# Kernel tuning notes

Hardware: AMD Instinct MI355X
Metric: run time of the kernel (lower is better)

## Reference

```python
import jax, jax.numpy as jnp
import numpy as np

B, S, D, H = 4, 1024, 1024, 16
HD = D // H  # head_dim = 64


def setup_inputs() -> dict:
    key = jax.random.key(0)
    ks = jax.random.split(key, 16)
    w = lambda k: jax.random.normal(k, (D, D), dtype=jnp.float32) * 0.02
    b = lambda k: jax.random.normal(k, (D,), dtype=jnp.float32) * 0.02
    x = jax.random.normal(ks[0], (B, S, D), dtype=jnp.float32)
    mask = jnp.tril(jnp.ones((S, S), dtype=jnp.int32))[None, None]  # causal [1,1,S,S]
    bar_indices = jax.random.randint(ks[1], (S,), 0, S, dtype=jnp.int64)
    beat_indices = jax.random.randint(ks[2], (S,), 0, S, dtype=jnp.int64)
    return {
        "x": x, "mask": mask, "bar_indices": bar_indices, "beat_indices": beat_indices,
        "Wq": w(ks[3]), "bq": b(ks[4]), "Wk": w(ks[5]), "bk": b(ks[6]),
        "Wv": w(ks[7]), "bv": b(ks[8]),
        "W_bark": w(ks[9]), "b_bark": b(ks[10]),
        "W_beatk": w(ks[11]), "b_beatk": b(ks[12]),
        "Wo": w(ks[13]), "bo": b(ks[14]),
    }


def reference(x, mask, bar_indices, beat_indices, Wq, bq, Wk, bk, Wv, bv,
              W_bark, b_bark, W_beatk, b_beatk, Wo, bo):
    Bs, Sl, Dm = x.shape
    heads, hd = H, Dm // H

    def proj(t, W, b):  # torch Linear: t @ W.T + b, then split heads -> [B,H,S,hd]
        y = t @ W.T + b
        return y.reshape(Bs, -1, heads, hd).transpose(0, 2, 1, 3)

    q = proj(x, Wq, bq)
    k = proj(x, Wk, bk)
    v = proj(x, Wv, bv)
    scale = 1.0 / jnp.sqrt(jnp.asarray(hd, x.dtype))

    scores = jnp.einsum('bhqd,bhkd->bhqk', q, k) * scale

    # hierarchical bar bias (bar_query is computed but unused in the original)
    bar_k = proj(x[:, bar_indices], W_bark, b_bark)
    scores = scores + 0.2 * (jnp.einsum('bhqd,bhkd->bhqk', q, bar_k) * scale)

    # hierarchical beat bias
    beat_k = proj(x[:, beat_indices], W_beatk, b_beatk)
    scores = scores + 0.1 * (jnp.einsum('bhqd,bhkd->bhqk', q, beat_k) * scale)

    scores = jnp.where(mask == 0, jnp.asarray(-1e9, scores.dtype), scores)
    attn = jax.nn.softmax(scores, axis=-1)  # dropout is identity in eval

    out = jnp.einsum('bhqk,bhkd->bhqd', attn, v)
    out = out.transpose(0, 2, 1, 3).reshape(Bs, Sl, Dm)
    return out @ Wo.T + bo
```

## Files before the change

kernel.cpp:

```cpp
#include <hip/hip_runtime.h>
#include <hip/hip_bf16.h>


typedef __bf16 bf16x8 __attribute__((ext_vector_type(8)));
typedef __bf16 bf16x4 __attribute__((ext_vector_type(4)));
typedef float  f32x4  __attribute__((ext_vector_type(4)));

#define DMODEL 1024

#define ASYNC_LOAD16(gp, lp)                                                  \
    __builtin_amdgcn_global_load_lds(                                         \
        (const __attribute__((address_space(1))) unsigned int*)(gp),          \
        (__attribute__((address_space(3))) unsigned int*)(lp), 16, 0, 0)

__global__ __launch_bounds__(256) void cvt_kernel(
    const float* __restrict__ x,
    const float* __restrict__ Wq, const float* __restrict__ Wk,
    const float* __restrict__ Wv, const float* __restrict__ Wbar,
    const float* __restrict__ Wbeat, const float* __restrict__ Wo,
    __bf16* __restrict__ dst)
{
    const int g = blockIdx.x * 256 + threadIdx.x;
    const size_t e = (size_t)g * 8;
    const int seg = (int)(e >> 20);
    const float* src; size_t off; float s = 1.0f;
    if (seg < 4)       { src = x;     off = e; }
    else if (seg == 4) { src = Wq;    off = e - ((size_t)4 << 20); }
    else if (seg == 5) { src = Wk;    off = e - ((size_t)5 << 20); }
    else if (seg == 6) { src = Wv;    off = e - ((size_t)6 << 20); }
    else if (seg == 7) { src = Wbar;  off = e - ((size_t)7 << 20); s = 0.2f; }
    else if (seg == 8) { src = Wbeat; off = e - ((size_t)8 << 20); s = 0.1f; }
    else               { src = Wo;    off = e - ((size_t)9 << 20); }
    const float4 a = *(const float4*)&src[off];
    const float4 b = *(const float4*)&src[off + 4];
    bf16x8 v;
    v[0] = (__bf16)(a.x * s); v[1] = (__bf16)(a.y * s);
    v[2] = (__bf16)(a.z * s); v[3] = (__bf16)(a.w * s);
    v[4] = (__bf16)(b.x * s); v[5] = (__bf16)(b.y * s);
    v[6] = (__bf16)(b.z * s); v[7] = (__bf16)(b.w * s);
    *(bf16x8*)&dst[e] = v;
}


#define SWZ_COL(r_, ks_) \
    (((((ks_) * 64) + quad * 16) ^ (((r_) & 7) << 4)) >> 1)

#define READ_ALL(c_)                                                          \
    do {                                                                      \
        _Pragma("unroll") for (int mh = 0; mh < 2; ++mh)                      \
        _Pragma("unroll") for (int mi = 0; mi < 2; ++mi) {                    \
            const int r_ = ((w >> 2) << 5) + mh * 64 + mi * 16 + l15;         \
            _Pragma("unroll") for (int ks = 0; ks < 2; ++ks)                  \
                af[mh][mi][ks] = *(const bf16x8*)&Alds[(c_) * 8192 +          \
                                        r_ * 64 + SWZ_COL(r_, ks)];           \
        }                                                                     \
        _Pragma("unroll") for (int nh = 0; nh < 2; ++nh)                      \
        _Pragma("unroll") for (int nj = 0; nj < 2; ++nj) {                    \
            const int r_ = ((w & 3) << 5) + nh * 128 + nj * 16 + l15;         \
            _Pragma("unroll") for (int ks = 0; ks < 2; ++ks)                  \
                bfr[nh][nj][ks] = *(const bf16x8*)&Blds[(c_) * 16384 +        \
                                        r_ * 64 + SWZ_COL(r_, ks)];           \
        }                                                                     \
    } while (0)

#define STAGE_A1(bufn_, h_, kt_)                                              \
    do {                                                                      \
        const int tm_ = (kt_) >> 4;                                           \
        const int k0_ = ((kt_) & 15) << 6;                                    \
        const __bf16* ap_ = (tm_ == 0) ? aA0##h_ : (tm_ == 1) ? aA1##h_       \
                                                              : aA2##h_;      \
        ASYNC_LOAD16(ap_ + k0_,                                               \
                     &Alds[(bufn_) * 8192 + (h_) * 4096 + w * 512]);          \
    } while (0)

#define STAGE_B2(bufn_, h_, kt_)                                              \
    do {                                                                      \
        const int tm_ = (kt_) >> 4;                                           \
        const int k0_ = ((kt_) & 15) << 6;                                    \
        const __bf16* wp_ = (tm_ == 0) ? W0 : (tm_ == 1) ? W1 : W2;           \
        ASYNC_LOAD16(wp_ + bro##h_##0 + k0_,                                  \
                     &Blds[(bufn_) * 16384 + (h_) * 8192 + w * 512]);         \
        ASYNC_LOAD16(wp_ + bro##h_##1 + k0_,                                  \
                     &Blds[(bufn_) * 16384 + (h_) * 8192 + 4096 + w * 512]);  \
    } while (0)

#define PHASE_BAR1()                                                          \
    do {                                                                      \
        __builtin_amdgcn_s_barrier();                                         \
        asm volatile("s_waitcnt lgkmcnt(0)" ::: "memory");                    \
    } while (0)

#define MFMA16(nh_)                                                           \
    do {                                                                      \
        __builtin_amdgcn_s_setprio(1);                                        \
        _Pragma("unroll") for (int mh = 0; mh < 2; ++mh)                      \
        _Pragma("unroll") for (int mi = 0; mi < 2; ++mi)                      \
        _Pragma("unroll") for (int nj = 0; nj < 2; ++nj)                      \
        _Pragma("unroll") for (int ks = 0; ks < 2; ++ks) {                    \
            acc[mh * 2 + mi][(nh_) * 2 + nj] =                                \
                __builtin_amdgcn_mfma_f32_16x16x32_bf16(                      \
                    af[mh][mi][ks], bfr[(nh_)][nj][ks],                       \
                    acc[mh * 2 + mi][(nh_) * 2 + nj], 0, 0, 0);               \
        }                                                                     \
        __builtin_amdgcn_s_setprio(0);                                        \
    } while (0)

__global__ __launch_bounds__(512, 2) void gemm8p_kernel(
    const __bf16* __restrict__ xb,
    const __bf16* __restrict__ Wqb, const __bf16* __restrict__ Wkb,
    const __bf16* __restrict__ Wvb, const __bf16* __restrict__ Wbarb,
    const __bf16* __restrict__ Wbeatb,
    const float* __restrict__ bq, const float* __restrict__ bk,
    const float* __restrict__ bv, const float* __restrict__ bbar,
    const float* __restrict__ bbeat,
    const int* __restrict__ bar_idx, const int* __restrict__ beat_idx,
    __bf16* __restrict__ qbuf, __bf16* __restrict__ keffbuf,
    __bf16* __restrict__ vtbuf)
{
    __shared__ __align__(16) __bf16 Alds[3 * 8192];
    __shared__ __align__(16) __bf16 Blds[3 * 16384];

    const int bid = blockIdx.x;
    int mode, tk;
    if (bid < 128)      { mode = 1; tk = bid; }
    else if (bid < 256) { mode = 0; tk = bid - 128; }
    else                { mode = 2; tk = bid - 256; }
    const int m0 = (tk >> 2) << 7;
    const int n0 = (tk & 3) << 8;
    const int nkt = (mode == 1) ? 48 : 16;

    const int t    = (int)threadIdx.x;
    const int w    = t >> 6;
    const int lane = t & 63;
    const int l15  = lane & 15;
    const int quad = lane >> 4;

    const int srow = t >> 3;
    const int scol = ((((t & 7) * 16) ^ (((t >> 3) & 7) << 4)) >> 1);

    const __bf16* aA00 = xb + (size_t)(m0 + srow) * DMODEL + scol;
    const __bf16* aA01 = xb + (size_t)(m0 + 64 + srow) * DMODEL + scol;
    const __bf16* aA10 = aA00; const __bf16* aA11 = aA01;
    const __bf16* aA20 = aA00; const __bf16* aA21 = aA01;
    const __bf16 *W0, *W1, *W2;
    if (mode == 0)      { W0 = W1 = W2 = Wqb; }
    else if (mode == 2) { W0 = W1 = W2 = Wvb; }
    else {
        W0 = Wkb; W1 = Wbarb; W2 = Wbeatb;
        const int bb = m0 & ~1023;
        const int lr = m0 & 1023;
        aA10 = xb + (size_t)(bb + bar_idx[lr + srow]) * DMODEL + scol;
        aA11 = xb + (size_t)(bb + bar_idx[lr + 64 + srow]) * DMODEL + scol;
        aA20 = xb + (size_t)(bb + beat_idx[lr + srow]) * DMODEL + scol;
        aA21 = xb + (size_t)(bb + beat_idx[lr + 64 + srow]) * DMODEL + scol;
    }
    const size_t bro00 = (size_t)(n0 + srow) * DMODEL + scol;
    const size_t bro01 = (size_t)(n0 + 64 + srow) * DMODEL + scol;
    const size_t bro10 = (size_t)(n0 + 128 + srow) * DMODEL + scol;
    const size_t bro11 = (size_t)(n0 + 192 + srow) * DMODEL + scol;

    f32x4 acc[4][4];
#pragma unroll
    for (int i = 0; i < 4; ++i)
#pragma unroll
        for (int j = 0; j < 4; ++j)
            acc[i][j] = {0.f, 0.f, 0.f, 0.f};
    bf16x8 af[2][2][2], bfr[2][2][2];

    STAGE_A1(0, 0, 0);
    STAGE_A1(0, 1, 0);
    STAGE_B2(0, 0, 0);
    STAGE_B2(0, 1, 0);
    asm volatile("" ::: "memory");
    STAGE_A1(1, 0, 1);
    STAGE_A1(1, 1, 1);
    STAGE_B2(1, 0, 1);
    STAGE_B2(1, 1, 1);
    asm volatile("s_waitcnt vmcnt(6)" ::: "memory");
    __builtin_amdgcn_s_barrier();

    int rc = 0, fc = 2;
#pragma unroll 1
    for (int kt = 0; kt < nkt; ++kt) {
        const int kn = kt + 2;
        const bool st = (kn < nkt);

        READ_ALL(rc);
        if (st) { STAGE_A1(fc, 0, kn); STAGE_A1(fc, 1, kn); }
        PHASE_BAR1();
        MFMA16(0);

        if (st) { STAGE_B2(fc, 0, kn); STAGE_B2(fc, 1, kn); }
        if (kt < nkt - 2)
            asm volatile("s_waitcnt vmcnt(6)" ::: "memory");
        else if (kt == nkt - 2)
            asm volatile("s_waitcnt vmcnt(0)" ::: "memory");
        PHASE_BAR1();
        MFMA16(1);

        rc = (rc == 2) ? 0 : rc + 1;
        fc = (fc == 2) ? 0 : fc + 1;
    }

#pragma unroll
    for (int an = 0; an < 4; ++an) {
        const int col = n0 + ((w & 3) << 5) + (an >> 1) * 128 +
                        (an & 1) * 16 + l15;
        float bias;
        if (mode == 0)      bias = bq[col];
        else if (mode == 1) bias = bk[col] + 0.2f * bbar[col] + 0.1f * bbeat[col];
        else                bias = bv[col];
#pragma unroll
        for (int am = 0; am < 4; ++am) {
            const int rowbase = m0 + ((w >> 2) << 5) + (am >> 1) * 64 +
                                (am & 1) * 16 + quad * 4;
            if (mode == 2) {
                const int bb = rowbase >> 10;
                const int sb = rowbase & 1023;
                bf16x4 vv;
#pragma unroll
                for (int r = 0; r < 4; ++r) vv[r] = (__bf16)(acc[am][an][r] + bias);
                *(bf16x4*)&vtbuf[((size_t)(bb * 1024 + col)) * 1024 + sb] = vv;
            } else if (mode == 0) {
#pragma unroll
                for (int r = 0; r < 4; ++r)
                    qbuf[(size_t)(rowbase + r) * DMODEL + col] =
                        (__bf16)((acc[am][an][r] + bias) * 0.125f);
            } else {
#pragma unroll
                for (int r = 0; r < 4; ++r)
                    keffbuf[(size_t)(rowbase + r) * DMODEL + col] =
                        (__bf16)(acc[am][an][r] + bias);
            }
        }
    }
}

__global__ __launch_bounds__(256) void oproj_kernel(
    const __bf16* __restrict__ attnb, const __bf16* __restrict__ Wob,
    const float* __restrict__ bo, float* __restrict__ outb)
{
    const int tile = blockIdx.x;
    const int m0 = (tile >> 3) << 6;
    const int n0 = (tile & 7) << 7;

    __shared__ __align__(16) __bf16 Alds[64 * 32];
    __shared__ __align__(16) __bf16 Blds[128 * 32];

    const int t    = threadIdx.x;
    const int w    = t >> 6;
    const int lane = t & 63;
    const int l15  = lane & 15;
    const int quad = lane >> 4;
    const int wm   = (w >> 1) << 5;
    const int wn   = (w & 1) << 6;
    const int srow = t >> 2;
    const int scol = ((((t & 3) * 16) ^ (((t >> 2) & 3) << 4)) >> 1);
    const int rcol = (((quad * 16) ^ ((l15 & 3) << 4)) >> 1);

    const __bf16* gA  = attnb + (size_t)(m0 + srow) * DMODEL + scol;
    const __bf16* gB0 = Wob + (size_t)(n0 + srow) * DMODEL + scol;
    const __bf16* gB1 = Wob + (size_t)(n0 + 64 + srow) * DMODEL + scol;
    __bf16* lA  = &Alds[w * 512];
    __bf16* lB0 = &Blds[w * 512];
    __bf16* lB1 = &Blds[2048 + w * 512];

    f32x4 acc[2][4];
    for (int i = 0; i < 2; ++i)
        for (int j = 0; j < 4; ++j)
            acc[i][j] = {0.f, 0.f, 0.f, 0.f};

    for (int kk = 0; kk < 32; ++kk) {
        const int k0 = kk * 32;
        ASYNC_LOAD16(gA + k0, lA);
        ASYNC_LOAD16(gB0 + k0, lB0);
        ASYNC_LOAD16(gB1 + k0, lB1);
        __syncthreads();

        bf16x8 af[2], bfr[4];
        for (int i = 0; i < 2; ++i)
            af[i] = *(const bf16x8*)&Alds[(wm + i * 16 + l15) * 32 + rcol];
        for (int j = 0; j < 4; ++j)
            bfr[j] = *(const bf16x8*)&Blds[(wn + j * 16 + l15) * 32 + rcol];

        for (int i = 0; i < 2; ++i)
            for (int j = 0; j < 4; ++j)
                acc[i][j] = __builtin_amdgcn_mfma_f32_16x16x32_bf16(
                    af[i], bfr[j], acc[i][j], 0, 0, 0);
        __syncthreads();
    }

    for (int j = 0; j < 4; ++j) {
        const int col = n0 + wn + j * 16 + l15;
        const float bias = bo[col];
        for (int i = 0; i < 2; ++i) {
            const int rowbase = m0 + wm + i * 16 + quad * 4;
            for (int r = 0; r < 4; ++r)
                outb[(size_t)(rowbase + r) * DMODEL + col] = acc[i][j][r] + bias;
        }
    }
}

__global__ __launch_bounds__(256) void attn_kernel(
    const __bf16* __restrict__ qbuf, const __bf16* __restrict__ keffbuf,
    const __bf16* __restrict__ vtbuf, __bf16* __restrict__ attnbuf)
{
    const int bh = blockIdx.y;
    const int b  = bh >> 4;
    const int h  = bh & 15;
    const int qt = blockIdx.x;
    const int q0 = qt * 64;

    __shared__ __align__(16) __bf16 Klds[64][72];
    __shared__ __align__(16) __bf16 Vlds[64][72];
    __shared__ __align__(16) __bf16 Plds[4][16][72];

    const int t    = threadIdx.x;
    const int w    = t >> 6;
    const int lane = t & 63;
    const int l15  = lane & 15;
    const int quad = lane >> 4;

    const __bf16* qbase =
        qbuf + (size_t)(b * 1024 + q0 + w * 16 + l15) * DMODEL + h * 64;
    bf16x8 qf0 = *(const bf16x8*)&qbase[quad * 8];
    bf16x8 qf1 = *(const bf16x8*)&qbase[32 + quad * 8];

    bf16x8 ones;
    for (int i = 0; i < 8; ++i) ones[i] = (__bf16)1.0f;

    f32x4 o[4];
    for (int i = 0; i < 4; ++i) o[i] = {0.f, 0.f, 0.f, 0.f};
    f32x4 lacc = {0.f, 0.f, 0.f, 0.f};

    const int srow = t >> 2;
    const int scol = (t & 3) * 16;

    const __bf16* kbase = keffbuf + (size_t)(b * 1024) * DMODEL + h * 64;
    const __bf16* vtb   = vtbuf + (size_t)(b * 1024 + h * 64) * 1024;

    for (int j = 0; j <= qt; ++j) {
        const __bf16* kg = kbase + (size_t)(j * 64 + srow) * DMODEL + scol;
        *(bf16x8*)&Klds[srow][scol]     = *(const bf16x8*)kg;
        *(bf16x8*)&Klds[srow][scol + 8] = *(const bf16x8*)(kg + 8);
        const __bf16* vg = vtb + (size_t)srow * 1024 + j * 64 + scol;
        *(bf16x8*)&Vlds[srow][scol]     = *(const bf16x8*)vg;
        *(bf16x8*)&Vlds[srow][scol + 8] = *(const bf16x8*)(vg + 8);
        __syncthreads();

        f32x4 sc[4];
        for (int nt = 0; nt < 4; ++nt) {
            sc[nt] = {0.f, 0.f, 0.f, 0.f};
            bf16x8 kf0 = *(const bf16x8*)&Klds[nt * 16 + l15][quad * 8];
            bf16x8 kf1 = *(const bf16x8*)&Klds[nt * 16 + l15][32 + quad * 8];
            sc[nt] = __builtin_amdgcn_mfma_f32_16x16x32_bf16(qf0, kf0, sc[nt], 0, 0, 0);
            sc[nt] = __builtin_amdgcn_mfma_f32_16x16x32_bf16(qf1, kf1, sc[nt], 0, 0, 0);
        }

        if (j == qt) {
            const int qrow_base = q0 + w * 16 + quad * 4;
            for (int nt = 0; nt < 4; ++nt) {
                const int kcol = j * 64 + nt * 16 + l15;
                for (int r = 0; r < 4; ++r)
                    if (kcol > qrow_base + r) sc[nt][r] = -1e30f;
            }
        }

        for (int nt = 0; nt < 4; ++nt)
            for (int r = 0; r < 4; ++r)
                sc[nt][r] = __expf(sc[nt][r]);

        for (int nt = 0; nt < 4; ++nt)
            for (int r = 0; r < 4; ++r)
                Plds[w][quad * 4 + r][nt * 16 + l15] = (__bf16)sc[nt][r];
        asm volatile("s_waitcnt lgkmcnt(0)" ::: "memory");

        bf16x8 pf0 = *(const bf16x8*)&Plds[w][l15][quad * 8];
        bf16x8 pf1 = *(const bf16x8*)&Plds[w][l15][32 + quad * 8];

        lacc = __builtin_amdgcn_mfma_f32_16x16x32_bf16(pf0, ones, lacc, 0, 0, 0);
        lacc = __builtin_amdgcn_mfma_f32_16x16x32_bf16(pf1, ones, lacc, 0, 0, 0);

        for (int nd = 0; nd < 4; ++nd) {
            bf16x8 vf0 = *(const bf16x8*)&Vlds[nd * 16 + l15][quad * 8];
            bf16x8 vf1 = *(const bf16x8*)&Vlds[nd * 16 + l15][32 + quad * 8];
            o[nd] = __builtin_amdgcn_mfma_f32_16x16x32_bf16(pf0, vf0, o[nd], 0, 0, 0);
            o[nd] = __builtin_amdgcn_mfma_f32_16x16x32_bf16(pf1, vf1, o[nd], 0, 0, 0);
        }
        __syncthreads();
    }

    float rinv[4];
    for (int r = 0; r < 4; ++r) rinv[r] = 1.0f / lacc[r];
    for (int nd = 0; nd < 4; ++nd) {
        for (int r = 0; r < 4; ++r) {
            const int row = q0 + w * 16 + quad * 4 + r;
            attnbuf[(size_t)(b * 1024 + row) * DMODEL + h * 64 + nd * 16 + l15] =
                (__bf16)(o[nd][r] * rinv[r]);
        }
    }
}

extern "C" void kernel_launch(void* const* d_in, const int* in_sizes, int n_in,
                              void* d_out, int out_size, void* d_ws, size_t ws_size,
                              hipStream_t stream) {
    const float* x     = (const float*)d_in[0];
    const int* bar     = (const int*)d_in[2];
    const int* beat    = (const int*)d_in[3];
    const float* Wq    = (const float*)d_in[4];
    const float* bq    = (const float*)d_in[5];
    const float* Wk    = (const float*)d_in[6];
    const float* bk    = (const float*)d_in[7];
    const float* Wv    = (const float*)d_in[8];
    const float* bv    = (const float*)d_in[9];
    const float* Wbar  = (const float*)d_in[10];
    const float* bbar  = (const float*)d_in[11];
    const float* Wbeat = (const float*)d_in[12];
    const float* bbeat = (const float*)d_in[13];
    const float* Wo    = (const float*)d_in[14];
    const float* bo    = (const float*)d_in[15];

    const size_t M1 = (size_t)1 << 20;
    __bf16* xb     = (__bf16*)d_ws;
    __bf16* Wqb    = xb + 4 * M1;
    __bf16* Wkb    = Wqb + M1;
    __bf16* Wvb    = Wkb + M1;
    __bf16* Wbarb  = Wvb + M1;
    __bf16* Wbeatb = Wbarb + M1;
    __bf16* Wob    = Wbeatb + M1;
    __bf16* qbuf   = Wob + M1;
    __bf16* keff   = qbuf + 4 * M1;
    __bf16* vt     = keff + 4 * M1;
    __bf16* attn   = vt + 4 * M1;
    float*  outb   = (float*)d_out;

    cvt_kernel<<<5120, 256, 0, stream>>>(x, Wq, Wk, Wv, Wbar, Wbeat, Wo, xb);

    gemm8p_kernel<<<384, 512, 0, stream>>>(
        xb, Wqb, Wkb, Wvb, Wbarb, Wbeatb,
        bq, bk, bv, bbar, bbeat, bar, beat,
        qbuf, keff, vt);

    attn_kernel<<<dim3(16, 64), 256, 0, stream>>>(qbuf, keff, vt, attn);

    oproj_kernel<<<512, 256, 0, stream>>>(attn, Wob, bo, outb);
}
```

Measured before the change: 221.5 us.

## Double-buffer attention K/V tiles with async LDS loads and 128-row query blocks

Rewrites the attention kernel to use 512-thread blocks covering 128 query rows, so each K/V tile loaded is shared by twice as many query rows. K/V tiles now go straight from global memory into LDS through global_load_lds, with two buffers so the next tile streams in while the current one is computed. The LDS layout uses an XOR swizzle to avoid bank conflicts. Blocks are ordered so heavy and light causal query tiles are interleaved across the grid. The trade-offs are more LDS per block, fewer blocks (512), and hand-placed waitcnt/barrier logic that must stay correct.

```diff
diff --git a/kernel.cpp b/kernel.cpp
--- a/kernel.cpp
+++ b/kernel.cpp
@@ -301,76 +301,98 @@
     }
 }
 
-__global__ __launch_bounds__(256) void attn_kernel(
+#define ATT_SLOT(q_, r_) ((((q_) ^ ((r_) & 7))) * 8)
+
+__global__ __launch_bounds__(512) void attn_kernel(
     const __bf16* __restrict__ qbuf, const __bf16* __restrict__ keffbuf,
     const __bf16* __restrict__ vtbuf, __bf16* __restrict__ attnbuf)
 {
-    const int bh = blockIdx.y;
+    const int id = blockIdx.x;
+    const int bh = id & 63;
     const int b  = bh >> 4;
     const int h  = bh & 15;
-    const int qt = blockIdx.x;
-    const int q0 = qt * 64;
-
-    __shared__ __align__(16) __bf16 Klds[64][72];
-    __shared__ __align__(16) __bf16 Vlds[64][72];
-    __shared__ __align__(16) __bf16 Plds[4][16][72];
-
-    const int t    = threadIdx.x;
+    const int qr = id >> 6;
+    const int qt = (qr < 4) ? qr : 11 - qr;
+    const int q0 = qt << 7;
+    const int NT = 2 * qt + 2;
+
+    __shared__ __align__(16) __bf16 Klds[2][64 * 64];
+    __shared__ __align__(16) __bf16 Vlds[2][64 * 64];
+    __shared__ __align__(16) __bf16 Plds[8][16][72];
+
+    const int t    = (int)threadIdx.x;
     const int w    = t >> 6;
     const int lane = t & 63;
     const int l15  = lane & 15;
     const int quad = lane >> 4;
 
+    const int srow = t >> 3;
+    const int scol = ((t & 7) ^ (srow & 7)) * 8;
+
+    const __bf16* gK = keffbuf + (size_t)(b * 1024 + srow) * DMODEL +
+                       h * 64 + scol;
+    const __bf16* gV = vtbuf + (size_t)(b * 1024 + h * 64 + srow) * 1024 +
+                       scol;
+
     const __bf16* qbase =
         qbuf + (size_t)(b * 1024 + q0 + w * 16 + l15) * DMODEL + h * 64;
     bf16x8 qf0 = *(const bf16x8*)&qbase[quad * 8];
     bf16x8 qf1 = *(const bf16x8*)&qbase[32 + quad * 8];
 
     bf16x8 ones;
+#pragma unroll
     for (int i = 0; i < 8; ++i) ones[i] = (__bf16)1.0f;
 
     f32x4 o[4];
+#pragma unroll
     for (int i = 0; i < 4; ++i) o[i] = {0.f, 0.f, 0.f, 0.f};
     f32x4 lacc = {0.f, 0.f, 0.f, 0.f};
 
-    const int srow = t >> 2;
-    const int scol = (t & 3) * 16;
-
-    const __bf16* kbase = keffbuf + (size_t)(b * 1024) * DMODEL + h * 64;
-    const __bf16* vtb   = vtbuf + (size_t)(b * 1024 + h * 64) * 1024;
-
-    for (int j = 0; j <= qt; ++j) {
-        const __bf16* kg = kbase + (size_t)(j * 64 + srow) * DMODEL + scol;
-        *(bf16x8*)&Klds[srow][scol]     = *(const bf16x8*)kg;
-        *(bf16x8*)&Klds[srow][scol + 8] = *(const bf16x8*)(kg + 8);
-        const __bf16* vg = vtb + (size_t)srow * 1024 + j * 64 + scol;
-        *(bf16x8*)&Vlds[srow][scol]     = *(const bf16x8*)vg;
-        *(bf16x8*)&Vlds[srow][scol + 8] = *(const bf16x8*)(vg + 8);
-        __syncthreads();
+    ASYNC_LOAD16(gK, &Klds[0][t * 8]);
+    ASYNC_LOAD16(gV, &Vlds[0][t * 8]);
+    asm volatile("" ::: "memory");
+    ASYNC_LOAD16(gK + (size_t)64 * DMODEL, &Klds[1][t * 8]);
+    ASYNC_LOAD16(gV + 64, &Vlds[1][t * 8]);
+    asm volatile("s_waitcnt vmcnt(2)" ::: "memory");
+    __builtin_amdgcn_s_barrier();
+
+#pragma unroll 1
+    for (int j = 0; j < NT; ++j) {
+        const int cur = j & 1;
 
         f32x4 sc[4];
+#pragma unroll
         for (int nt = 0; nt < 4; ++nt) {
+            const int row = nt * 16 + l15;
+            bf16x8 kf0 = *(const bf16x8*)&Klds[cur][row * 64 +
+                                                    ATT_SLOT(quad, row)];
+            bf16x8 kf1 = *(const bf16x8*)&Klds[cur][row * 64 +
+                                                    ATT_SLOT(quad + 4, row)];
             sc[nt] = {0.f, 0.f, 0.f, 0.f};
-            bf16x8 kf0 = *(const bf16x8*)&Klds[nt * 16 + l15][quad * 8];
-            bf16x8 kf1 = *(const bf16x8*)&Klds[nt * 16 + l15][32 + quad * 8];
             sc[nt] = __builtin_amdgcn_mfma_f32_16x16x32_bf16(qf0, kf0, sc[nt], 0, 0, 0);
             sc[nt] = __builtin_amdgcn_mfma_f32_16x16x32_bf16(qf1, kf1, sc[nt], 0, 0, 0);
         }
 
-        if (j == qt) {
+        if (j >= NT - 2) {
             const int qrow_base = q0 + w * 16 + quad * 4;
+#pragma unroll
             for (int nt = 0; nt < 4; ++nt) {
                 const int kcol = j * 64 + nt * 16 + l15;
+#pragma unroll
                 for (int r = 0; r < 4; ++r)
                     if (kcol > qrow_base + r) sc[nt][r] = -1e30f;
             }
         }
 
+#pragma unroll
         for (int nt = 0; nt < 4; ++nt)
+#pragma unroll
             for (int r = 0; r < 4; ++r)
                 sc[nt][r] = __expf(sc[nt][r]);
 
+#pragma unroll
         for (int nt = 0; nt < 4; ++nt)
+#pragma unroll
             for (int r = 0; r < 4; ++r)
                 Plds[w][quad * 4 + r][nt * 16 + l15] = (__bf16)sc[nt][r];
         asm volatile("s_waitcnt lgkmcnt(0)" ::: "memory");
@@ -381,18 +403,37 @@
         lacc = __builtin_amdgcn_mfma_f32_16x16x32_bf16(pf0, ones, lacc, 0, 0, 0);
         lacc = __builtin_amdgcn_mfma_f32_16x16x32_bf16(pf1, ones, lacc, 0, 0, 0);
 
+#pragma unroll
         for (int nd = 0; nd < 4; ++nd) {
-            bf16x8 vf0 = *(const bf16x8*)&Vlds[nd * 16 + l15][quad * 8];
-            bf16x8 vf1 = *(const bf16x8*)&Vlds[nd * 16 + l15][32 + quad * 8];
+            const int row = nd * 16 + l15;
+            bf16x8 vf0 = *(const bf16x8*)&Vlds[cur][row * 64 +
+                                                    ATT_SLOT(quad, row)];
+            bf16x8 vf1 = *(const bf16x8*)&Vlds[cur][row * 64 +
+                                                    ATT_SLOT(quad + 4, row)];
             o[nd] = __builtin_amdgcn_mfma_f32_16x16x32_bf16(pf0, vf0, o[nd], 0, 0, 0);
             o[nd] = __builtin_amdgcn_mfma_f32_16x16x32_bf16(pf1, vf1, o[nd], 0, 0, 0);
         }
+
         __syncthreads();
+        if (j + 2 < NT) {
+            ASYNC_LOAD16(gK + (size_t)(j + 2) * 64 * DMODEL, &Klds[cur][t * 8]);
+            ASYNC_LOAD16(gV + (size_t)(j + 2) * 64, &Vlds[cur][t * 8]);
+        }
+        if (j + 1 < NT) {
+            if (j + 2 < NT)
+                asm volatile("s_waitcnt vmcnt(2)" ::: "memory");
+            else
+                asm volatile("s_waitcnt vmcnt(0)" ::: "memory");
+            __builtin_amdgcn_s_barrier();
+        }
     }
 
     float rinv[4];
+#pragma unroll
     for (int r = 0; r < 4; ++r) rinv[r] = 1.0f / lacc[r];
+#pragma unroll
     for (int nd = 0; nd < 4; ++nd) {
+#pragma unroll
         for (int r = 0; r < 4; ++r) {
             const int row = q0 + w * 16 + quad * 4 + r;
             attnbuf[(size_t)(b * 1024 + row) * DMODEL + h * 64 + nd * 16 + l15] =
@@ -441,7 +482,7 @@
         bq, bk, bv, bbar, bbeat, bar, beat,
         qbuf, keff, vt);
 
-    attn_kernel<<<dim3(16, 64), 256, 0, stream>>>(qbuf, keff, vt, attn);
+    attn_kernel<<<512, 512, 0, stream>>>(qbuf, keff, vt, attn);
 
     oproj_kernel<<<512, 256, 0, stream>>>(attn, Wob, bo, outb);
 }
```

After: 205.5 us. 1.08x faster.
